# Kernel optimization log

Hardware: AMD Instinct MI355X
Metric: run time of the kernel (lower is better)

The kernel has to match this reference:

```python
import math
import jax, jax.numpy as jnp
import numpy as np

NUM_HEADS = 16
QUERY_SIZE = 1024
SEQ = 2048
HEAD = QUERY_SIZE // NUM_HEADS  # qk_size = vo_size = 64


def setup_inputs() -> dict:
    key = jax.random.key(0)
    ks = jax.random.split(key, 8)
    s = 0.02
    query = jax.random.normal(ks[0], (SEQ, QUERY_SIZE), jnp.float32)
    key_ = jax.random.normal(ks[1], (SEQ, QUERY_SIZE), jnp.float32)
    value = jax.random.normal(ks[2], (SEQ, QUERY_SIZE), jnp.float32)
    # causal mask (mask='causal' with state=None -> offset 0)
    mask = jnp.tril(jnp.ones((SEQ, SEQ), dtype=bool))
    Wq = jax.random.normal(ks[3], (QUERY_SIZE, QUERY_SIZE), jnp.float32) * s
    Wk = jax.random.normal(ks[4], (QUERY_SIZE, QUERY_SIZE), jnp.float32) * s
    Wv = jax.random.normal(ks[5], (QUERY_SIZE, QUERY_SIZE), jnp.float32) * s
    Wo = jax.random.normal(ks[6], (QUERY_SIZE, QUERY_SIZE), jnp.float32) * s
    return {"query": query, "key_": key_, "value": value, "mask": mask,
            "Wq": Wq, "Wk": Wk, "Wv": Wv, "Wo": Wo}


def reference(query, key_, value, mask, Wq, Wk, Wv, Wo):
    H, D = NUMS = NUM_HEADS, HEAD
    S = query.shape[0]
    inv_sqrt_d = 1.0 / math.sqrt(D)
    # per-token linear projections, split into heads: [S, H, D]
    q = (query @ Wq.T).reshape(S, H, D)
    k = (key_ @ Wk.T).reshape(S, H, D)
    v = (value @ Wv.T).reshape(S, H, D)
    # NOTE: original divides BOTH q and k by sqrt(d) (effective 1/d scaling)
    q = q * inv_sqrt_d
    k = k * inv_sqrt_d
    # logits per head: [H, S, S]
    logits = jnp.einsum('shd,Shd->hsS', q, k)
    logits = jnp.where(mask[None, :, :], logits, jnp.finfo(logits.dtype).min)
    # per-head GLOBAL max subtraction, softmax in fp32, cast back (faithful)
    m = jnp.max(logits, axis=(1, 2), keepdims=True)
    weights = jax.nn.softmax((logits - m).astype(jnp.float32), axis=-1).astype(query.dtype)
    attn = jnp.einsum('hsS,ShD->shD', weights, v).reshape(S, H * D)
    return attn @ Wo.T
```

## Files before the change

kernel.cpp:

```cpp
#include <hip/hip_runtime.h>
#include <hip/hip_bf16.h>

typedef __bf16 bf16_t;
typedef __bf16 bf16x8 __attribute__((ext_vector_type(8)));
typedef float f32x4 __attribute__((ext_vector_type(4)));
typedef float f32x16 __attribute__((ext_vector_type(16)));

#define MFMA(A, B, C) __builtin_amdgcn_mfma_f32_16x16x32_bf16(A, B, C, 0, 0, 0)
#define MFMA32(A, B, C) __builtin_amdgcn_mfma_f32_32x32x16_bf16(A, B, C, 0, 0, 0)

#define GLL16(g, l) __builtin_amdgcn_global_load_lds(                      \
    (const __attribute__((address_space(1))) void*)(g),                    \
    (__attribute__((address_space(3))) void*)(l), 16, 0, 0)

static __device__ __forceinline__ bf16x8 frag4(unsigned a, unsigned b, unsigned c, unsigned d) {
  union { unsigned u[4]; bf16x8 v; } x;
  x.u[0] = a; x.u[1] = b; x.u[2] = c; x.u[3] = d;
  return x.v;
}
static __device__ __forceinline__ unsigned pack2b(bf16_t lo, bf16_t hi) {
  union { bf16_t b[2]; unsigned u; } x;
  x.b[0] = lo; x.b[1] = hi;
  return x.u;
}

__global__ __launch_bounds__(256) void cvt_all(
    const float* __restrict__ q, const float* __restrict__ k, const float* __restrict__ v,
    const float* __restrict__ wq, const float* __restrict__ wk,
    const float* __restrict__ wv, const float* __restrict__ wo,
    bf16_t* __restrict__ xq, bf16_t* __restrict__ xk, bf16_t* __restrict__ xv,
    bf16_t* __restrict__ ywq, bf16_t* __restrict__ ywk,
    bf16_t* __restrict__ ywv, bf16_t* __restrict__ ywo)
{
  const long gid = (long)blockIdx.x * 256 + threadIdx.x;
  const float* s; bf16_t* d; long off; float sc = 1.0f;
  if (gid < 262144)       { s = q;  d = xq;  off = gid; }
  else if (gid < 524288)  { s = k;  d = xk;  off = gid - 262144; }
  else if (gid < 786432)  { s = v;  d = xv;  off = gid - 524288; }
  else if (gid < 917504)  { s = wq; d = ywq; off = gid - 786432;  sc = 0.125f; }
  else if (gid < 1048576) { s = wk; d = ywk; off = gid - 917504;  sc = 0.125f * 1.44269504f; }
  else if (gid < 1179648) { s = wv; d = ywv; off = gid - 1048576; }
  else                    { s = wo; d = ywo; off = gid - 1179648; }
  const float* p = s + off * 8;
  float4 a = *(const float4*)p, b = *(const float4*)(p + 4);
  bf16x8 o;
  o[0] = (bf16_t)(a.x * sc); o[1] = (bf16_t)(a.y * sc);
  o[2] = (bf16_t)(a.z * sc); o[3] = (bf16_t)(a.w * sc);
  o[4] = (bf16_t)(b.x * sc); o[5] = (bf16_t)(b.y * sc);
  o[6] = (bf16_t)(b.z * sc); o[7] = (bf16_t)(b.w * sc);
  *(bf16x8*)(d + off * 8) = o;
}

__device__ __forceinline__ void gemm_core(const bf16_t* __restrict__ A,
                                          const bf16_t* __restrict__ W,
                                          int bm, int bn,
                                          bf16_t (&As)[2][128 * 64],
                                          bf16_t (&Bs)[2][64 * 64],
                                          f32x4 (&acc)[4][2])
{
  const int tid = threadIdx.x, lane = tid & 63, wave = tid >> 6;
  const int l15 = lane & 15, l4 = lane >> 4, l7 = l15 & 7;
  const int wm = (wave >> 1) * 64, wn = (wave & 1) * 32;

  auto stage = [&](int buf, int k0) {
#pragma unroll
    for (int i = 0; i < 4; ++i) {
      const int id = i * 256 + tid, row = id >> 3, cph = id & 7;
      GLL16(A + (size_t)(bm + row) * 1024 + k0 + 8 * (cph ^ (row & 7)),
            &As[buf][(i * 256 + wave * 64) * 8]);
    }
#pragma unroll
    for (int i = 0; i < 2; ++i) {
      const int id = i * 256 + tid, row = id >> 3, cph = id & 7;
      GLL16(W + (size_t)(bn + row) * 1024 + k0 + 8 * (cph ^ (row & 7)),
            &Bs[buf][(i * 256 + wave * 64) * 8]);
    }
  };

  stage(0, 0);
#pragma unroll
  for (int s = 0; s < 16; ++s) {
    if (s + 1 < 16) stage((s + 1) & 1, (s + 1) * 64);
    __syncthreads();
    const bf16_t* as = As[s & 1];
    const bf16_t* bs = Bs[s & 1];
#pragma unroll
    for (int ks = 0; ks < 2; ++ks) {
      bf16x8 af[4], bfr[2];
#pragma unroll
      for (int i = 0; i < 4; ++i)
        af[i] = *(const bf16x8*)(&as[(wm + i * 16 + l15) * 64 + 8 * ((ks * 4 + l4) ^ l7)]);
#pragma unroll
      for (int j = 0; j < 2; ++j)
        bfr[j] = *(const bf16x8*)(&bs[(wn + j * 16 + l15) * 64 + 8 * ((ks * 4 + l4) ^ l7)]);
#pragma unroll
      for (int i = 0; i < 4; ++i)
#pragma unroll
        for (int j = 0; j < 2; ++j)
          acc[i][j] = MFMA(af[i], bfr[j], acc[i][j]);
    }
    __syncthreads();
  }
}

__global__ __launch_bounds__(256) void gemm_qkv(
    const bf16_t* __restrict__ xq, const bf16_t* __restrict__ xk, const bf16_t* __restrict__ xv,
    const bf16_t* __restrict__ ywq, const bf16_t* __restrict__ ywk, const bf16_t* __restrict__ ywv,
    bf16_t* __restrict__ qo, bf16_t* __restrict__ ko, bf16_t* __restrict__ vt)
{
  __shared__ __align__(16) bf16_t As[2][128 * 64];
  __shared__ __align__(16) bf16_t Bs[2][64 * 64];
  const int z = blockIdx.z;
  const bf16_t* A = z == 0 ? xq : z == 1 ? xk : xv;
  const bf16_t* W = z == 0 ? ywq : z == 1 ? ywk : ywv;
  const int bm = blockIdx.x * 128, bn = blockIdx.y * 64;
  f32x4 acc[4][2] = {};
  gemm_core(A, W, bm, bn, As, Bs, acc);
  const int tid = threadIdx.x, lane = tid & 63, wave = tid >> 6;
  const int l15 = lane & 15, l4 = lane >> 4;
  const int wm = (wave >> 1) * 64, wn = (wave & 1) * 32;
  if (z < 2) {
    bf16_t* C = z == 0 ? qo : ko;
#pragma unroll
    for (int i = 0; i < 4; ++i)
#pragma unroll
      for (int j = 0; j < 2; ++j)
#pragma unroll
        for (int r = 0; r < 4; ++r)
          C[(size_t)(bm + wm + i * 16 + 4 * l4 + r) * 1024 + bn + wn + j * 16 + l15] =
              (bf16_t)acc[i][j][r];
  } else {
#pragma unroll
    for (int i = 0; i < 4; ++i)
#pragma unroll
      for (int j = 0; j < 2; ++j)
#pragma unroll
        for (int r = 0; r < 4; ++r)
          vt[(size_t)(bn + wn + j * 16 + l15) * 2048 + bm + wm + i * 16 + 4 * l4 + r] =
              (bf16_t)acc[i][j][r];
  }
}

__global__ __launch_bounds__(256) void gemm_out(
    const bf16_t* __restrict__ ctx, const bf16_t* __restrict__ ywo, float* __restrict__ out)
{
  __shared__ __align__(16) bf16_t As[2][128 * 64];
  __shared__ __align__(16) bf16_t Bs[2][64 * 64];
  const int bm = blockIdx.x * 128, bn = blockIdx.y * 64;
  f32x4 acc[4][2] = {};
  gemm_core(ctx, ywo, bm, bn, As, Bs, acc);
  const int tid = threadIdx.x, lane = tid & 63, wave = tid >> 6;
  const int l15 = lane & 15, l4 = lane >> 4;
  const int wm = (wave >> 1) * 64, wn = (wave & 1) * 32;
#pragma unroll
  for (int i = 0; i < 4; ++i)
#pragma unroll
    for (int j = 0; j < 2; ++j)
#pragma unroll
      for (int r = 0; r < 4; ++r)
        out[(size_t)(bm + wm + i * 16 + 4 * l4 + r) * 1024 + bn + wn + j * 16 + l15] =
            acc[i][j][r];
}

__global__ __launch_bounds__(256) void attn_reg(
    const bf16_t* __restrict__ Qb, const bf16_t* __restrict__ Kb,
    const bf16_t* __restrict__ Vt, bf16_t* __restrict__ Ctx)
{
  __shared__ float Osc[3][32 * 64];
  __shared__ float Dsc[4][32];

  const int bid = blockIdx.x;
  const int u = 63 - (bid >> 4);
  const int h = bid & 15;
  const int hoff = h * 64;
  const int lane = threadIdx.x & 63, tph = threadIdx.x >> 6;
  const int l31 = lane & 31, hi = lane >> 5;

  const int qb = u * 32;
  const int q_lane = qb + l31;
  const int nch = u + 1;
  const bf16_t* Kh = Kb + hoff;
  const bf16_t* Vh = Vt + (size_t)hoff * 2048;

  bf16x8 qf[4];
#pragma unroll
  for (int st = 0; st < 4; ++st)
    qf[st] = *(const bf16x8*)(Qb + (size_t)(qb + l31) * 1024 + hoff + 16 * st + 8 * hi);

  f32x16 o0 = {}, o1 = {};
  float den = 0.f;

  bf16x8 kfA[4], vfA[4], kfB[4], vfB[4];
  auto LOAD = [&](bf16x8 (&kf)[4], bf16x8 (&vf)[4], int c) {
    const int t0 = c * 32;
#pragma unroll
    for (int st = 0; st < 4; ++st)
      kf[st] = *(const bf16x8*)(Kh + (size_t)(t0 + l31) * 1024 + 16 * st + 8 * hi);
#pragma unroll
    for (int db = 0; db < 2; ++db)
#pragma unroll
      for (int kh = 0; kh < 2; ++kh)
        vf[db * 2 + kh] = *(const bf16x8*)(Vh + (size_t)(32 * db + l31) * 2048 + t0 + 16 * kh + 8 * hi);
  };

  auto PROC = [&](const bf16x8 (&kf)[4], const bf16x8 (&vf)[4], int c) {
    const int t0 = c * 32;
    f32x16 sv = {};
#pragma unroll
    for (int st = 0; st < 4; ++st)
      sv = MFMA32(kf[st], qf[st], sv);
    const bool diag = (c + 1 == nch);
    bf16_t pb[16];
#pragma unroll
    for (int reg = 0; reg < 16; ++reg) {
      const int t = t0 + (reg & 3) + 8 * (reg >> 2) + 4 * hi;
      float e = __builtin_amdgcn_exp2f(sv[reg]);
      if (diag && t > q_lane) e = 0.f;
      const bf16_t b = (bf16_t)e;
      pb[reg] = b;
      den += (float)b;
    }
    unsigned pk[8];
#pragma unroll
    for (int i = 0; i < 8; ++i) pk[i] = pack2b(pb[2 * i], pb[2 * i + 1]);
    const unsigned r0a = __shfl_xor((int)(hi ? pk[0] : pk[2]), 32, 64);
    const unsigned r0b = __shfl_xor((int)(hi ? pk[1] : pk[3]), 32, 64);
    const unsigned r1a = __shfl_xor((int)(hi ? pk[4] : pk[6]), 32, 64);
    const unsigned r1b = __shfl_xor((int)(hi ? pk[5] : pk[7]), 32, 64);
    const bf16x8 pf0 = hi ? frag4(r0a, r0b, pk[2], pk[3]) : frag4(pk[0], pk[1], r0a, r0b);
    const bf16x8 pf1 = hi ? frag4(r1a, r1b, pk[6], pk[7]) : frag4(pk[4], pk[5], r1a, r1b);
    o0 = MFMA32(pf0, vf[0], o0);
    o0 = MFMA32(pf1, vf[1], o0);
    o1 = MFMA32(pf0, vf[2], o1);
    o1 = MFMA32(pf1, vf[3], o1);
  };

  int c = tph;
  if (c < nch) {
    LOAD(kfA, vfA, c);
    while (true) {
      if (c + 4 < nch) LOAD(kfB, vfB, c + 4);
      PROC(kfA, vfA, c);
      c += 4;
      if (c >= nch) break;
      if (c + 4 < nch) LOAD(kfA, vfA, c + 4);
      PROC(kfB, vfB, c);
      c += 4;
      if (c >= nch) break;
    }
  }

  den += __shfl_xor(den, 32, 64);

  if (hi == 0) Dsc[tph][l31] = den;
  if (tph > 0) {
#pragma unroll
    for (int reg = 0; reg < 16; ++reg) {
      const int qr = (reg & 3) + 8 * (reg >> 2) + 4 * hi;
      Osc[tph - 1][qr * 64 + l31] = o0[reg];
      Osc[tph - 1][qr * 64 + 32 + l31] = o1[reg];
    }
  }
  __syncthreads();
  if (tph == 0) {
    const float dtot = Dsc[0][l31] + Dsc[1][l31] + Dsc[2][l31] + Dsc[3][l31];
    if (hi == 0) Dsc[0][l31] = dtot;
    asm volatile("s_waitcnt lgkmcnt(0)" ::: "memory");
    __builtin_amdgcn_sched_barrier(0);
#pragma unroll
    for (int reg = 0; reg < 16; ++reg) {
      const int qr = (reg & 3) + 8 * (reg >> 2) + 4 * hi;
      const float s0 = o0[reg] + Osc[0][qr * 64 + l31] + Osc[1][qr * 64 + l31] + Osc[2][qr * 64 + l31];
      const float s1 = o1[reg] + Osc[0][qr * 64 + 32 + l31] + Osc[1][qr * 64 + 32 + l31] + Osc[2][qr * 64 + 32 + l31];
      const float inv = 1.0f / Dsc[0][qr];
      Ctx[(size_t)(qb + qr) * 1024 + hoff + l31] = (bf16_t)(s0 * inv);
      Ctx[(size_t)(qb + qr) * 1024 + hoff + 32 + l31] = (bf16_t)(s1 * inv);
    }
  }
}

extern "C" void kernel_launch(void* const* d_in, const int* in_sizes, int n_in,
                              void* d_out, int out_size, void* d_ws, size_t ws_size,
                              hipStream_t stream)
{
  const float* query = (const float*)d_in[0];
  const float* key_  = (const float*)d_in[1];
  const float* value = (const float*)d_in[2];
  const float* Wq = (const float*)d_in[4];
  const float* Wk = (const float*)d_in[5];
  const float* Wv = (const float*)d_in[6];
  const float* Wo = (const float*)d_in[7];
  float* out = (float*)d_out;

  const size_t SE = (size_t)2048 * 1024, EE = (size_t)1024 * 1024;
  bf16_t* xq  = (bf16_t*)d_ws;
  bf16_t* xk  = xq + SE;
  bf16_t* xv  = xk + SE;
  bf16_t* wq  = xv + SE;
  bf16_t* wk  = wq + EE;
  bf16_t* wv  = wk + EE;
  bf16_t* wo  = wv + EE;
  bf16_t* qo  = wo + EE;
  bf16_t* ko  = qo + SE;
  bf16_t* vt  = ko + SE;
  bf16_t* ctx = vt + SE;

  cvt_all<<<5120, 256, 0, stream>>>(query, key_, value, Wq, Wk, Wv, Wo,
                                    xq, xk, xv, wq, wk, wv, wo);
  gemm_qkv<<<dim3(16, 16, 3), 256, 0, stream>>>(xq, xk, xv, wq, wk, wv, qo, ko, vt);
  attn_reg<<<1024, 256, 0, stream>>>(qo, ko, vt, ctx);
  gemm_out<<<dim3(16, 16), 256, 0, stream>>>(ctx, wo, out);
}
```

Before: 85.89 us.

## Pair causal query tiles per block and stage K/V through swizzled LDS

Replaces the per-32-row attention kernel with 256 blocks of 512 threads. Each block handles two 64-row query tiles taken from opposite ends of the causal triangle (jp and 31-jp) so every block does a similar amount of work. K/V chunks of 128 keys are loaded cooperatively into double-buffered XOR-swizzled shared memory, and both query tiles reuse each chunk, which cuts redundant global reads of K and V. The trade-offs are fewer, larger blocks (256 on the device), a block-wide barrier every chunk, 64KB of LDS that limits occupancy, and waves that idle on chunks above the diagonal.

```diff
diff --git a/kernel.cpp b/kernel.cpp
--- a/kernel.cpp
+++ b/kernel.cpp
@@ -162,60 +162,80 @@
             acc[i][j][r];
 }
 
-__global__ __launch_bounds__(256) void attn_reg(
+__global__ __launch_bounds__(512) void attn_pair(
     const bf16_t* __restrict__ Qb, const bf16_t* __restrict__ Kb,
     const bf16_t* __restrict__ Vt, bf16_t* __restrict__ Ctx)
 {
-  __shared__ float Osc[3][32 * 64];
-  __shared__ float Dsc[4][32];
+  __shared__ __align__(16) char pool[64 * 1024];
+  bf16_t* KsP = (bf16_t*)pool;
+  bf16_t* VsP = (bf16_t*)(pool + 32768);
+  float*  Osc = (float*)pool;
+  float*  Dsc = (float*)(pool + 49152);
 
   const int bid = blockIdx.x;
-  const int u = 63 - (bid >> 4);
-  const int h = bid & 15;
+  const int h = bid & 15, jp = bid >> 4;
   const int hoff = h * 64;
-  const int lane = threadIdx.x & 63, tph = threadIdx.x >> 6;
-  const int l31 = lane & 31, hi = lane >> 5;
-
-  const int qb = u * 32;
-  const int q_lane = qb + l31;
-  const int nch = u + 1;
-  const bf16_t* Kh = Kb + hoff;
-  const bf16_t* Vh = Vt + (size_t)hoff * 2048;
-
-  bf16x8 qf[4];
-#pragma unroll
-  for (int st = 0; st < 4; ++st)
-    qf[st] = *(const bf16x8*)(Qb + (size_t)(qb + l31) * 1024 + hoff + 16 * st + 8 * hi);
-
-  f32x16 o0 = {}, o1 = {};
-  float den = 0.f;
-
-  bf16x8 kfA[4], vfA[4], kfB[4], vfB[4];
-  auto LOAD = [&](bf16x8 (&kf)[4], bf16x8 (&vf)[4], int c) {
-    const int t0 = c * 32;
-#pragma unroll
-    for (int st = 0; st < 4; ++st)
-      kf[st] = *(const bf16x8*)(Kh + (size_t)(t0 + l31) * 1024 + 16 * st + 8 * hi);
-#pragma unroll
-    for (int db = 0; db < 2; ++db)
-#pragma unroll
-      for (int kh = 0; kh < 2; ++kh)
-        vf[db * 2 + kh] = *(const bf16x8*)(Vh + (size_t)(32 * db + l31) * 2048 + t0 + 16 * kh + 8 * hi);
-  };
-
-  auto PROC = [&](const bf16x8 (&kf)[4], const bf16x8 (&vf)[4], int c) {
-    const int t0 = c * 32;
+  const int tid = threadIdx.x, lane = tid & 63, wave = tid >> 6;
+  const int qs = wave & 1, tw = wave >> 1;
+  const int l31 = lane & 31, hi = lane >> 5, l7 = l31 & 7;
+
+  const int qtA = jp, qtB = 31 - jp;
+  const int qbA = qtA * 64, qbB = qtB * 64;
+  const int nsc = (qtB * 64 + 63) / 128 + 1;
+
+  bf16x8 qfA[4], qfB[4];
+#pragma unroll
+  for (int st = 0; st < 4; ++st) {
+    qfA[st] = *(const bf16x8*)(Qb + (size_t)(qbA + 32 * qs + l31) * 1024 + hoff + 16 * st + 8 * hi);
+    qfB[st] = *(const bf16x8*)(Qb + (size_t)(qbB + 32 * qs + l31) * 1024 + hoff + 16 * st + 8 * hi);
+  }
+
+  f32x16 oA0 = {}, oA1 = {}, oB0 = {}, oB1 = {};
+  float dA = 0.f, dB = 0.f;
+
+  bf16x8 rk[2], rv[2];
+  auto issue = [&](int c) {
+    const int t0 = c * 128;
+#pragma unroll
+    for (int i = 0; i < 2; ++i) {
+      const int id = tid + 512 * i;
+      const int kr = id >> 3, kc = id & 7;
+      rk[i] = *(const bf16x8*)(Kb + (size_t)(t0 + kr) * 1024 + hoff + 8 * kc);
+      const int vr = id >> 4, vc = id & 15;
+      rv[i] = *(const bf16x8*)(Vt + (size_t)(hoff + vr) * 2048 + t0 + 8 * vc);
+    }
+  };
+  auto commit = [&](int buf) {
+#pragma unroll
+    for (int i = 0; i < 2; ++i) {
+      const int id = tid + 512 * i;
+      const int kr = id >> 3, kc = id & 7;
+      *(bf16x8*)(&KsP[buf * 8192 + kr * 64 + 8 * (kc ^ (kr & 7))]) = rk[i];
+      const int vr = id >> 4, vc = id & 15;
+      *(bf16x8*)(&VsP[buf * 8192 + vr * 128 + 8 * (vc ^ (vr & 7))]) = rv[i];
+    }
+  };
+
+  auto PROC = [&](int cur, int c, int qb, const bf16x8 (&qf)[4],
+                  f32x16& o0, f32x16& o1, float& den) {
+    const int qg0 = qb + 32 * qs;
+    const int t0w = 128 * c + 32 * tw;
+    if (t0w > qg0 + 31) return;
+    const bf16_t* Ksb = KsP + cur * 8192;
+    const bf16_t* Vsb = VsP + cur * 8192;
     f32x16 sv = {};
 #pragma unroll
-    for (int st = 0; st < 4; ++st)
-      sv = MFMA32(kf[st], qf[st], sv);
-    const bool diag = (c + 1 == nch);
+    for (int st = 0; st < 4; ++st) {
+      bf16x8 kf = *(const bf16x8*)(&Ksb[(32 * tw + l31) * 64 + 8 * ((2 * st + hi) ^ l7)]);
+      sv = MFMA32(kf, qf[st], sv);
+    }
+    const bool diag = (t0w == qg0);
     bf16_t pb[16];
 #pragma unroll
     for (int reg = 0; reg < 16; ++reg) {
-      const int t = t0 + (reg & 3) + 8 * (reg >> 2) + 4 * hi;
+      const int tpat = (reg & 3) + 8 * (reg >> 2) + 4 * hi;
       float e = __builtin_amdgcn_exp2f(sv[reg]);
-      if (diag && t > q_lane) e = 0.f;
+      if (diag && tpat > l31) e = 0.f;
       const bf16_t b = (bf16_t)e;
       pb[reg] = b;
       den += (float)b;
@@ -229,54 +249,67 @@
     const unsigned r1b = __shfl_xor((int)(hi ? pk[5] : pk[7]), 32, 64);
     const bf16x8 pf0 = hi ? frag4(r0a, r0b, pk[2], pk[3]) : frag4(pk[0], pk[1], r0a, r0b);
     const bf16x8 pf1 = hi ? frag4(r1a, r1b, pk[6], pk[7]) : frag4(pk[4], pk[5], r1a, r1b);
-    o0 = MFMA32(pf0, vf[0], o0);
-    o0 = MFMA32(pf1, vf[1], o0);
-    o1 = MFMA32(pf0, vf[2], o1);
-    o1 = MFMA32(pf1, vf[3], o1);
-  };
-
-  int c = tph;
-  if (c < nch) {
-    LOAD(kfA, vfA, c);
-    while (true) {
-      if (c + 4 < nch) LOAD(kfB, vfB, c + 4);
-      PROC(kfA, vfA, c);
-      c += 4;
-      if (c >= nch) break;
-      if (c + 4 < nch) LOAD(kfA, vfA, c + 4);
-      PROC(kfB, vfB, c);
-      c += 4;
-      if (c >= nch) break;
-    }
+    bf16x8 vf00 = *(const bf16x8*)(&Vsb[(l31) * 128 + 8 * ((4 * tw + hi) ^ l7)]);
+    bf16x8 vf01 = *(const bf16x8*)(&Vsb[(l31) * 128 + 8 * ((4 * tw + 2 + hi) ^ l7)]);
+    bf16x8 vf10 = *(const bf16x8*)(&Vsb[(32 + l31) * 128 + 8 * ((4 * tw + hi) ^ l7)]);
+    bf16x8 vf11 = *(const bf16x8*)(&Vsb[(32 + l31) * 128 + 8 * ((4 * tw + 2 + hi) ^ l7)]);
+    o0 = MFMA32(pf0, vf00, o0);
+    o0 = MFMA32(pf1, vf01, o0);
+    o1 = MFMA32(pf0, vf10, o1);
+    o1 = MFMA32(pf1, vf11, o1);
+  };
+
+  issue(0);
+  commit(0);
+  int cur = 0;
+  for (int c = 0; c < nsc; ++c) {
+    const bool pre = (c + 1 < nsc);
+    if (pre) issue(c + 1);
+    __syncthreads();
+    PROC(cur, c, qbB, qfB, oB0, oB1, dB);
+    PROC(cur, c, qbA, qfA, oA0, oA1, dA);
+    if (pre) commit(cur ^ 1);
+    cur ^= 1;
   }
 
-  den += __shfl_xor(den, 32, 64);
-
-  if (hi == 0) Dsc[tph][l31] = den;
-  if (tph > 0) {
-#pragma unroll
-    for (int reg = 0; reg < 16; ++reg) {
-      const int qr = (reg & 3) + 8 * (reg >> 2) + 4 * hi;
-      Osc[tph - 1][qr * 64 + l31] = o0[reg];
-      Osc[tph - 1][qr * 64 + 32 + l31] = o1[reg];
-    }
-  }
-  __syncthreads();
-  if (tph == 0) {
-    const float dtot = Dsc[0][l31] + Dsc[1][l31] + Dsc[2][l31] + Dsc[3][l31];
-    if (hi == 0) Dsc[0][l31] = dtot;
-    asm volatile("s_waitcnt lgkmcnt(0)" ::: "memory");
-    __builtin_amdgcn_sched_barrier(0);
-#pragma unroll
-    for (int reg = 0; reg < 16; ++reg) {
-      const int qr = (reg & 3) + 8 * (reg >> 2) + 4 * hi;
-      const float s0 = o0[reg] + Osc[0][qr * 64 + l31] + Osc[1][qr * 64 + l31] + Osc[2][qr * 64 + l31];
-      const float s1 = o1[reg] + Osc[0][qr * 64 + 32 + l31] + Osc[1][qr * 64 + 32 + l31] + Osc[2][qr * 64 + 32 + l31];
-      const float inv = 1.0f / Dsc[0][qr];
-      Ctx[(size_t)(qb + qr) * 1024 + hoff + l31] = (bf16_t)(s0 * inv);
-      Ctx[(size_t)(qb + qr) * 1024 + hoff + 32 + l31] = (bf16_t)(s1 * inv);
-    }
-  }
+  dA += __shfl_xor(dA, 32, 64);
+  dB += __shfl_xor(dB, 32, 64);
+
+  auto combine = [&](int qb, const f32x16& o0, const f32x16& o1, float den) {
+    __syncthreads();
+    if (hi == 0) Dsc[(tw * 2 + qs) * 32 + l31] = den;
+    if (tw > 0) {
+#pragma unroll
+      for (int reg = 0; reg < 16; ++reg) {
+        const int qr = (reg & 3) + 8 * (reg >> 2) + 4 * hi;
+        Osc[((tw - 1) * 2 + qs) * 2048 + qr * 64 + l31] = o0[reg];
+        Osc[((tw - 1) * 2 + qs) * 2048 + qr * 64 + 32 + l31] = o1[reg];
+      }
+    }
+    __syncthreads();
+    if (tw == 0) {
+      const float dtot = Dsc[(0 * 2 + qs) * 32 + l31] + Dsc[(1 * 2 + qs) * 32 + l31] +
+                         Dsc[(2 * 2 + qs) * 32 + l31] + Dsc[(3 * 2 + qs) * 32 + l31];
+      if (hi == 0) Dsc[qs * 32 + l31] = dtot;
+      asm volatile("s_waitcnt lgkmcnt(0)" ::: "memory");
+      __builtin_amdgcn_sched_barrier(0);
+#pragma unroll
+      for (int reg = 0; reg < 16; ++reg) {
+        const int qr = (reg & 3) + 8 * (reg >> 2) + 4 * hi;
+        const float inv = 1.0f / Dsc[qs * 32 + qr];
+        const float s0 = o0[reg] + Osc[(0 * 2 + qs) * 2048 + qr * 64 + l31] +
+                                   Osc[(1 * 2 + qs) * 2048 + qr * 64 + l31] +
+                                   Osc[(2 * 2 + qs) * 2048 + qr * 64 + l31];
+        const float s1 = o1[reg] + Osc[(0 * 2 + qs) * 2048 + qr * 64 + 32 + l31] +
+                                   Osc[(1 * 2 + qs) * 2048 + qr * 64 + 32 + l31] +
+                                   Osc[(2 * 2 + qs) * 2048 + qr * 64 + 32 + l31];
+        Ctx[(size_t)(qb + 32 * qs + qr) * 1024 + hoff + l31] = (bf16_t)(s0 * inv);
+        Ctx[(size_t)(qb + 32 * qs + qr) * 1024 + hoff + 32 + l31] = (bf16_t)(s1 * inv);
+      }
+    }
+  };
+  combine(qbA, oA0, oA1, dA);
+  combine(qbB, oB0, oB1, dB);
 }
 
 extern "C" void kernel_launch(void* const* d_in, const int* in_sizes, int n_in,
@@ -308,6 +341,6 @@
   cvt_all<<<5120, 256, 0, stream>>>(query, key_, value, Wq, Wk, Wv, Wo,
                                     xq, xk, xv, wq, wk, wv, wo);
   gemm_qkv<<<dim3(16, 16, 3), 256, 0, stream>>>(xq, xk, xv, wq, wk, wv, qo, ko, vt);
-  attn_reg<<<1024, 256, 0, stream>>>(qo, ko, vt, ctx);
+  attn_pair<<<256, 512, 0, stream>>>(qo, ko, vt, ctx);
   gemm_out<<<dim3(16, 16), 256, 0, stream>>>(ctx, wo, out);
 }
```

After: 73.23 us. 1.17x faster.
